# Optimization experiments

Hardware: AMD Instinct MI355X
Metric: run time of the kernel (lower is better)

## Reference

```python
import jax, jax.numpy as jnp
import numpy as np

B, L, D = 256, 256, 128          # batch, max_len, embedding_dim
H = W = 16                       # H=int(sqrt(L)), W=L//H
N, CBD = 128, 1024               # embedding_num, code_book_dim = N*8 = D*8
BETA = 0.25
BN_EPS = 1e-3                    # tf.layers.batch_normalization default


def _conv(x, w, b):
    return jax.lax.conv_general_dilated(x, w, (1, 1), 'VALID',
        dimension_numbers=('NHWC', 'HWIO', 'NHWC')) + b


def _convT(x, w, b):
    return jax.lax.conv_transpose(x, w, (1, 1), 'VALID',
        dimension_numbers=('NHWC', 'HWIO', 'NHWC')) + b


def _bn(x, g, b):
    # inference-mode BN with moving_mean=0, moving_var=1 (tf.layers default training=False)
    return g * (x * (1.0 / np.sqrt(1.0 + BN_EPS))) + b


def setup_inputs() -> dict:
    key = jax.random.key(0)
    ks = jax.random.split(key, 24)
    rn = lambda k, s, sc=0.05: (jax.random.normal(k, s, dtype=jnp.float32) * sc)
    inp = {
        'x': jax.random.normal(ks[0], (B, L, D), dtype=jnp.float32),
        'mask': jnp.ones((B, L), dtype=jnp.float32),
        'code_book': jax.random.normal(ks[1], (N, CBD), dtype=jnp.float32),
        # encoder: conv2d k=2 valid, channels D -> 2D -> 4D -> 8D
        'ew1': rn(ks[2], (2, 2, D, 2 * D)), 'eb1': jnp.zeros((2 * D,), jnp.float32),
        'eg1': jnp.ones((2 * D,), jnp.float32), 'ebt1': jnp.zeros((2 * D,), jnp.float32),
        'ew2': rn(ks[3], (2, 2, 2 * D, 4 * D)), 'eb2': jnp.zeros((4 * D,), jnp.float32),
        'eg2': jnp.ones((4 * D,), jnp.float32), 'ebt2': jnp.zeros((4 * D,), jnp.float32),
        'ew3': rn(ks[4], (2, 2, 4 * D, 8 * D)), 'eb3': jnp.zeros((8 * D,), jnp.float32),
        # decoder: conv2d_transpose k=2 valid, channels 8D -> 4D -> 2D -> D
        'dw1': rn(ks[5], (2, 2, 8 * D, 4 * D)), 'db1': jnp.zeros((4 * D,), jnp.float32),
        'dg1': jnp.ones((4 * D,), jnp.float32), 'dbt1': jnp.zeros((4 * D,), jnp.float32),
        'dw2': rn(ks[6], (2, 2, 4 * D, 2 * D)), 'db2': jnp.zeros((2 * D,), jnp.float32),
        'dg2': jnp.ones((2 * D,), jnp.float32), 'dbt2': jnp.zeros((2 * D,), jnp.float32),
        'dw3': rn(ks[7], (2, 2, 2 * D, D)), 'db3': jnp.zeros((D,), jnp.float32),
    }
    return inp


def reference(x, mask, code_book,
              ew1, eb1, eg1, ebt1, ew2, eb2, eg2, ebt2, ew3, eb3,
              dw1, db1, dg1, dbt1, dw2, db2, dg2, dbt2, dw3, db3):
    # ---- encoder (conv branch) ----
    xi = x.reshape(-1, H, W, D)                                   # [B,16,16,D]
    h = jax.nn.relu(_bn(_conv(xi, ew1, eb1), eg1, ebt1))          # [B,15,15,2D]
    h = jax.nn.relu(_bn(_conv(h, ew2, eb2), eg2, ebt2))           # [B,14,14,4D]
    x_encode = _conv(h, ew3, eb3)                                 # [B,13,13,8D]

    # ---- VQ codebook lookup (get_quantized) ----
    flat = x_encode.reshape(-1, CBD)                              # [B*169, CBD]
    dist = (jnp.sum(flat ** 2, axis=1, keepdims=True)
            + jnp.sum(code_book ** 2, axis=1)
            - 2.0 * flat @ code_book.T)                           # [B*169, N]
    idx = jnp.argmin(dist, axis=1)
    quantized = code_book[idx].reshape(x_encode.shape)            # gather == one_hot @ code_book

    # ---- straight-through + decoder ----
    ste = x_encode + jax.lax.stop_gradient(quantized - x_encode)
    h = jax.nn.relu(_bn(_convT(ste, dw1, db1), dg1, dbt1))        # [B,14,14,4D]
    h = jax.nn.relu(_bn(_convT(h, dw2, db2), dg2, dbt2))          # [B,15,15,2D]
    vq = _convT(h, dw3, db3)                                      # [B,16,16,D]
    vq_x = vq.reshape(-1, L, D)

    vq_mean = jnp.sum(vq_x, axis=1) / jnp.sum(mask, axis=-1, keepdims=True)

    recon = jnp.mean((x - vq_x) ** 2)
    vq_l = jnp.mean((quantized - jax.lax.stop_gradient(x_encode)) ** 2)
    commit = jnp.mean((x_encode - jax.lax.stop_gradient(quantized)) ** 2)
    vqvae_loss = recon + vq_l + BETA * commit
    return (vq_mean, vq_x, x_encode, quantized, vqvae_loss)
```

## Files before the change

### kernel.cpp

```cpp
#include <hip/hip_runtime.h>
#include <math.h>

typedef float f4 __attribute__((ext_vector_type(4)));
typedef short s8 __attribute__((ext_vector_type(8)));

#define WS_FLOATS 66000000L
__device__ float g_fallback[WS_FLOATS];

__device__ __forceinline__ f4 ldg4(const float* p) { return *(const f4*)p; }

__device__ __forceinline__ unsigned short bfr(float x) {
    unsigned int u = __float_as_uint(x);
    u += 0x7fffu + ((u >> 16) & 1u);
    return (unsigned short)(u >> 16);
}
__device__ __forceinline__ float bff(unsigned short h) {
    return __uint_as_float(((unsigned int)h) << 16);
}
__device__ __forceinline__ s8 z8() { s8 z = {0,0,0,0,0,0,0,0}; return z; }

__device__ __forceinline__ void split8(const f4& x0, const f4& x1, s8& hi, s8& lo) {
#pragma unroll
    for (int e = 0; e < 4; ++e) {
        unsigned short h0 = bfr(x0[e]);
        hi[e] = (short)h0; lo[e] = (short)bfr(x0[e] - bff(h0));
        unsigned short h1 = bfr(x1[e]);
        hi[e + 4] = (short)h1; lo[e + 4] = (short)bfr(x1[e] - bff(h1));
    }
}

template<int EPI>
__global__ __launch_bounds__(512, 2)
void gemm256(const short* __restrict__ aSrc, const short* __restrict__ wHi,
             const float* __restrict__ bias, const float* __restrict__ gamma,
             const float* __restrict__ beta, void* __restrict__ oHi,
             double* __restrict__ sacc, const short* __restrict__ zsrc,
             int IH, int IW, int OHOW, int OW, int N, int K, int off,
             int ntShift, float bns)
{
    extern __shared__ short smem[];

    const int tid = threadIdx.x;
    const int w = tid >> 6;
    const int l = tid & 63;
    const int lr = l >> 3;
    const int lc = l & 7;
    const int fr = l & 15, fq = l >> 4;
    const int wm = (w >> 2) * 128;
    const int wn = (w & 3) * 64;

    int m0, n0;
    {
        const int nwg = gridDim.x;
        const int bid = blockIdx.x;
        const int q = nwg >> 3, r = nwg & 7;
        const int xcd = bid & 7, c = bid >> 3;
        const int wg = (xcd < r ? xcd * (q + 1) : r * (q + 1) + (xcd - r) * q) + c;
        const int NTm1 = (1 << ntShift) - 1;
        m0 = (wg >> ntShift) * 256;
        n0 = (wg & NTm1) * 256;
    }

    int bOff[4], oiA[4], ojA[4], bRowB[4];
#pragma unroll
    for (int i = 0; i < 4; ++i) {
        int row = (w << 5) + (i << 3) + lr;
        int m = m0 + row;
        int b = m / OHOW; int rem = m - b * OHOW;
        oiA[i] = rem / OW; ojA[i] = rem - oiA[i] * OW;
        bOff[i] = b * IH * IW;
        bRowB[i] = (n0 + row) * K;
    }
    const int swz = (lc ^ lr) << 3;

    auto stage = [&](int sel, int kc) {
        short* Ab = smem + sel * 16384;
        short* Bb = smem + 32768 + sel * 16384;
        const int t = kc >> 9;
        const int ci = (kc & 511) + swz;
        const int di = (t >> 1) + off, dj = (t & 1) + off;
#pragma unroll
        for (int i = 0; i < 4; ++i) {
            int ii = oiA[i] + di, jj = ojA[i] + dj;
            bool v = (ii >= 0) && (ii < IH) && (jj >= 0) && (jj < IW);
            const short* sA = v ? aSrc + (long)(bOff[i] + ii * IW + jj) * 512 + ci
                                : zsrc + (l << 3);
            __builtin_amdgcn_global_load_lds(
                (const __attribute__((address_space(1))) void*)sA,
                (__attribute__((address_space(3))) void*)(Ab + (((w << 5) + (i << 3)) * 64)),
                16, 0, 0);
            const short* sB = wHi + bRowB[i] + kc + swz;
            __builtin_amdgcn_global_load_lds(
                (const __attribute__((address_space(1))) void*)sB,
                (__attribute__((address_space(3))) void*)(Bb + (((w << 5) + (i << 3)) * 64)),
                16, 0, 0);
        }
    };

    f4 acc[8][4];
#pragma unroll
    for (int a = 0; a < 8; ++a)
#pragma unroll
        for (int b = 0; b < 4; ++b) acc[a][b] = (f4){0.f, 0.f, 0.f, 0.f};

    const int NT = K >> 6;
    stage(0, 0);
    stage(1, 64);

    for (int t = 0; t < NT; ++t) {
        const int sel = t & 1;
        const short* Ab = smem + sel * 16384;
        const short* Bb = smem + 32768 + sel * 16384;

        if (t < NT - 1) asm volatile("s_waitcnt vmcnt(8)" ::: "memory");
        else            asm volatile("s_waitcnt vmcnt(0)" ::: "memory");
        __builtin_amdgcn_s_barrier();
        __builtin_amdgcn_sched_barrier(0);

        s8 af[8], bf[4];
#pragma unroll
        for (int mf = 0; mf < 8; ++mf) {
            int row = wm + mf * 16 + fr;
            int c = fq ^ (row & 7);
            af[mf] = *(const s8*)&Ab[row * 64 + (c << 3)];
        }
#pragma unroll
        for (int nf = 0; nf < 4; ++nf) {
            int row = wn + nf * 16 + fr;
            int c = fq ^ (row & 7);
            bf[nf] = *(const s8*)&Bb[row * 64 + (c << 3)];
        }
        asm volatile("s_waitcnt lgkmcnt(0)" ::: "memory");
        __builtin_amdgcn_sched_barrier(0);
        __builtin_amdgcn_s_setprio(1);
#pragma unroll
        for (int mf = 0; mf < 8; ++mf)
#pragma unroll
            for (int nf = 0; nf < 4; ++nf)
                acc[mf][nf] = __builtin_amdgcn_mfma_f32_16x16x32_bf16(
                    af[mf], bf[nf], acc[mf][nf], 0, 0, 0);
        __builtin_amdgcn_s_setprio(0);

#pragma unroll
        for (int mf = 0; mf < 8; ++mf) {
            int row = wm + mf * 16 + fr;
            int c = (4 + fq) ^ (row & 7);
            af[mf] = *(const s8*)&Ab[row * 64 + (c << 3)];
        }
#pragma unroll
        for (int nf = 0; nf < 4; ++nf) {
            int row = wn + nf * 16 + fr;
            int c = (4 + fq) ^ (row & 7);
            bf[nf] = *(const s8*)&Bb[row * 64 + (c << 3)];
        }
        asm volatile("s_waitcnt lgkmcnt(0)" ::: "memory");
        __builtin_amdgcn_sched_barrier(0);
        __builtin_amdgcn_s_barrier();
        __builtin_amdgcn_sched_barrier(0);
        if (t + 2 < NT) stage(sel, (t + 2) << 6);

        __builtin_amdgcn_s_setprio(1);
#pragma unroll
        for (int mf = 0; mf < 8; ++mf)
#pragma unroll
            for (int nf = 0; nf < 4; ++nf)
                acc[mf][nf] = __builtin_amdgcn_mfma_f32_16x16x32_bf16(
                    af[mf], bf[nf], acc[mf][nf], 0, 0, 0);
        __builtin_amdgcn_s_setprio(0);
    }

    if (EPI == 3) {
        float bi[4];
#pragma unroll
        for (int nf = 0; nf < 4; ++nf) bi[nf] = bias[n0 + wn + nf * 16 + fr];
        double tsum = 0.0;
#pragma unroll
        for (int mf = 0; mf < 8; ++mf)
#pragma unroll
            for (int j = 0; j < 4; ++j) {
                long gm = m0 + wm + mf * 16 + fq * 4 + j;
                float* orow = (float*)oHi + gm * (long)N + n0;
#pragma unroll
                for (int nf = 0; nf < 4; ++nf) {
                    float v = acc[mf][nf][j] + bi[nf];
                    orow[wn + nf * 16 + fr] = v;
                    tsum += (double)v * v;
                }
            }
        __syncthreads();
        double* rd = (double*)smem;
        rd[tid] = tsum; __syncthreads();
        for (int h = 256; h; h >>= 1) {
            if (tid < h) rd[tid] += rd[tid + h];
            __syncthreads();
        }
        if (tid == 0) atomicAdd(sacc, rd[0]);
    } else {
        float bi[4], ga[4], be[4];
#pragma unroll
        for (int nf = 0; nf < 4; ++nf) {
            int col = n0 + wn + nf * 16 + fr;
            bi[nf] = bias[col]; ga[nf] = gamma[col]; be[nf] = beta[col];
        }
#pragma unroll
        for (int mf = 0; mf < 8; ++mf)
#pragma unroll
            for (int j = 0; j < 4; ++j) {
                long gm = m0 + wm + mf * 16 + fq * 4 + j;
                short* orow = (short*)oHi + gm * (long)N + n0;
#pragma unroll
                for (int nf = 0; nf < 4; ++nf) {
                    float v = ga[nf] * ((acc[mf][nf][j] + bi[nf]) * bns) + be[nf];
                    orow[wn + nf * 16 + fr] = (short)bfr(fmaxf(v, 0.f));
                }
            }
    }
}

template<int SPLIT, int ASRC, int EPI, int OUTF>
__global__ __launch_bounds__(256, 2)
void mfma_conv(const void* __restrict__ aHi, const void* __restrict__ aLo,
               const short* __restrict__ wHi, const short* __restrict__ wLo,
               const float* __restrict__ bias, const float* __restrict__ gamma,
               const float* __restrict__ beta,
               void* __restrict__ oHi, void* __restrict__ oLo,
               int* __restrict__ idxo,
               const float* __restrict__ xref, float* __restrict__ colsum,
               double* __restrict__ sacc,
               int IH, int IW, int Cin, int cinShift, int OHOW, int OW,
               int N, int K, int off, int ntShift, float bns)
{
    constexpr int PL = 128 * 64;
    constexpr int NPL = (SPLIT == 1) ? 3 : 4;
    __shared__ short smem[NPL * PL];
    short* Ah = smem;
    short* Al  = smem + PL;
    short* BhS = smem + 2 * PL;
    short* BlS = smem + 3 * PL;

    const int tid = threadIdx.x;
    const int lane = tid & 63, wid = tid >> 6;
    const int fr = lane & 15, fq = lane >> 4;
    const int wm = (wid >> 1) * 64, wn = (wid & 1) * 64;

    int m0, n0;
    {
        const int nwg = gridDim.x;
        const int bid = blockIdx.x;
        const int q = nwg >> 3, r = nwg & 7;
        const int xcd = bid & 7, c = bid >> 3;
        const int wg = (xcd < r ? xcd * (q + 1) : r * (q + 1) + (xcd - r) * q) + c;
        const int NTm1 = (1 << ntShift) - 1;
        m0 = (wg >> ntShift) * 128;
        n0 = (wg & NTm1) * 128;
    }

    const int sr = tid >> 1;
    const int skh = (tid & 1) << 5;

    long tapOff[4]; bool tv[4];
    {
        int m = m0 + sr;
        int b = m / OHOW; int rem = m - b * OHOW;
        int oi = rem / OW; int oj = rem - oi * OW;
#pragma unroll
        for (int t = 0; t < 4; ++t) {
            int ii = oi + (t >> 1) + off, jj = oj + (t & 1) + off;
            bool v = (ii >= 0) && (ii < IH) && (jj >= 0) && (jj < IW);
            tv[t] = v;
            tapOff[t] = ((long)b * IH + (v ? ii : 0)) * IW + (v ? jj : 0);
        }
    }

    f4 acc[4][4];
#pragma unroll
    for (int a = 0; a < 4; ++a)
#pragma unroll
        for (int b = 0; b < 4; ++b) acc[a][b] = (f4){0.f, 0.f, 0.f, 0.f};

    const short* wHrow = wHi + (long)(n0 + sr) * K;
    const short* wLrow = (SPLIT == 2) ? (wLo + (long)(n0 + sr) * K) : nullptr;

    const int swzW = (sr & 7) << 3;
    const int sbase = sr * 64;

    s8 rah[4], ral[4], rbh[4], rbl[4];
    f4 rax0[4], rax1[4];

    auto LOADREGS = [&](int kc) {
        const int kk = kc + skh;
        const int t = kk >> cinShift;
        const int ci = kk & (Cin - 1);
        const bool v = tv[t];
        if (ASRC == 0) {
            const float* p = (const float*)aHi + tapOff[t] * Cin + ci;
#pragma unroll
            for (int q = 0; q < 4; ++q) {
                rax0[q] = v ? ldg4(p + 8 * q) : (f4){0.f,0.f,0.f,0.f};
                rax1[q] = v ? ldg4(p + 8 * q + 4) : (f4){0.f,0.f,0.f,0.f};
            }
        } else if (ASRC == 1) {
            const short* ph = (const short*)aHi + tapOff[t] * Cin + ci;
            const short* pl = (const short*)aLo + tapOff[t] * Cin + ci;
#pragma unroll
            for (int q = 0; q < 4; ++q) {
                rah[q] = v ? *(const s8*)(ph + 8 * q) : z8();
                ral[q] = v ? *(const s8*)(pl + 8 * q) : z8();
            }
        } else {
            const short* ph = (const short*)aHi + tapOff[t] * Cin + ci;
#pragma unroll
            for (int q = 0; q < 4; ++q) rah[q] = v ? *(const s8*)(ph + 8 * q) : z8();
        }
        if (SPLIT == 2) {
#pragma unroll
            for (int q = 0; q < 4; ++q) {
                rbh[q] = *(const s8*)(wHrow + kc + skh + 8 * q);
                rbl[q] = *(const s8*)(wLrow + kc + skh + 8 * q);
            }
        }
    };

    auto STORE = [&]() {
        if (ASRC == 0) {
#pragma unroll
            for (int q = 0; q < 4; ++q) split8(rax0[q], rax1[q], rah[q], ral[q]);
        }
#pragma unroll
        for (int q = 0; q < 4; ++q) {
            int kx = (skh + 8 * q) ^ swzW;
            *(s8*)&Ah[sbase + kx] = rah[q];
            if (SPLIT == 2) {
                *(s8*)&Al[sbase + kx]  = ral[q];
                *(s8*)&BhS[sbase + kx] = rbh[q];
                *(s8*)&BlS[sbase + kx] = rbl[q];
            }
        }
    };

    auto stageB = [&](int bsel, int kc2) {
        short* bb = smem + (1 + bsel) * PL;
        const int rr0 = wid << 5;
#pragma unroll
        for (int i = 0; i < 4; ++i) {
            const int r = rr0 + 8 * i + (lane >> 3);
            const int c = lane & 7;
            const short* src = wHi + (long)(n0 + r) * K + kc2 + 8 * (c ^ (r & 7));
            __builtin_amdgcn_global_load_lds(
                (const __attribute__((address_space(1))) void*)src,
                (__attribute__((address_space(3))) void*)(bb + (rr0 + 8 * i) * 64),
                16, 0, 0);
        }
    };

    int bcur = 0;
    LOADREGS(0);
    if (SPLIT == 1) stageB(0, 0);

    for (int kc = 0; kc < K; kc += 64) {
        if (SPLIT == 1) {
            asm volatile("s_waitcnt lgkmcnt(0)" ::: "memory");
            __builtin_amdgcn_s_barrier();
            STORE();
            if (kc + 64 < K) {
                stageB(bcur ^ 1, kc + 64);
                asm volatile("s_waitcnt vmcnt(4)" ::: "memory");
            } else {
                asm volatile("s_waitcnt vmcnt(0)" ::: "memory");
            }
            __builtin_amdgcn_sched_barrier(0);
            asm volatile("s_waitcnt lgkmcnt(0)" ::: "memory");
            __builtin_amdgcn_s_barrier();
        } else {
            __syncthreads();
            STORE();
            __syncthreads();
        }
        if (kc + 64 < K) LOADREGS(kc + 64);

        const short* Bc = (SPLIT == 1) ? (smem + (1 + bcur) * PL) : BhS;

        __builtin_amdgcn_s_setprio(1);
#pragma unroll
        for (int ks = 0; ks < 2; ++ks) {
            const int colk = ks * 32 + fq * 8;
            s8 afh[4], afl[4], bfh[4], bfl[4];
#pragma unroll
            for (int mf = 0; mf < 4; ++mf) {
                int ar = wm + mf * 16 + fr;
                int ai = ar * 64 + (colk ^ ((ar & 7) << 3));
                afh[mf] = *(const s8*)&Ah[ai];
                if (SPLIT == 2) afl[mf] = *(const s8*)&Al[ai];
            }
#pragma unroll
            for (int nf = 0; nf < 4; ++nf) {
                int br = wn + nf * 16 + fr;
                int bi2 = br * 64 + (colk ^ ((br & 7) << 3));
                bfh[nf] = *(const s8*)&Bc[bi2];
                if (SPLIT == 2) bfl[nf] = *(const s8*)&BlS[bi2];
            }
#pragma unroll
            for (int mf = 0; mf < 4; ++mf)
#pragma unroll
                for (int nf = 0; nf < 4; ++nf) {
                    acc[mf][nf] = __builtin_amdgcn_mfma_f32_16x16x32_bf16(
                        afh[mf], bfh[nf], acc[mf][nf], 0, 0, 0);
                    if (SPLIT == 2) {
                        acc[mf][nf] = __builtin_amdgcn_mfma_f32_16x16x32_bf16(
                            afh[mf], bfl[nf], acc[mf][nf], 0, 0, 0);
                        acc[mf][nf] = __builtin_amdgcn_mfma_f32_16x16x32_bf16(
                            afl[mf], bfh[nf], acc[mf][nf], 0, 0, 0);
                    }
                }
        }
        __builtin_amdgcn_s_setprio(0);
        bcur ^= 1;
    }

    if (EPI == 2) {
        __syncthreads();
        float* pbv = (float*)smem;
        int*   piv = (int*)((float*)smem + 256);
        float cnv[4];
#pragma unroll
        for (int nf = 0; nf < 4; ++nf) cnv[nf] = bias[n0 + wn + nf * 16 + fr];
#pragma unroll
        for (int mf = 0; mf < 4; ++mf)
#pragma unroll
            for (int j = 0; j < 4; ++j) {
                float best = 3.4e38f; int bi = 0;
#pragma unroll
                for (int nf = 0; nf < 4; ++nf) {
                    float d = cnv[nf] - 2.0f * acc[mf][nf][j];
                    int col = wn + nf * 16 + fr;
                    if (d < best) { best = d; bi = col; }
                }
#pragma unroll
                for (int sh = 1; sh <= 8; sh <<= 1) {
                    float ov = __shfl_xor(best, sh, 64);
                    int ob = __shfl_xor(bi, sh, 64);
                    if (ov < best || (ov == best && ob < bi)) { best = ov; bi = ob; }
                }
                if (fr == 0) {
                    int r = wm + mf * 16 + fq * 4 + j;
                    pbv[(wid & 1) * 128 + r] = best;
                    piv[(wid & 1) * 128 + r] = bi;
                }
            }
        __syncthreads();
        double win = 0.0;
        if (tid < 128) {
            float b0 = pbv[tid], b1 = pbv[128 + tid];
            int i0 = piv[tid], i1 = piv[128 + tid];
            idxo[m0 + tid] = (b1 < b0) ? i1 : i0;
            win = (double)((b1 < b0) ? b1 : b0);
        }
        __syncthreads();
        double* rd = (double*)smem;
        rd[tid] = win; __syncthreads();
        for (int h = 128; h; h >>= 1) {
            if (tid < h) rd[tid] += rd[tid + h];
            __syncthreads();
        }
        if (tid == 0) atomicAdd(sacc, rd[0]);
        return;
    }

    float bi[4], ga[4], be[4];
#pragma unroll
    for (int nf = 0; nf < 4; ++nf) {
        int col = n0 + wn + nf * 16 + fr;
        bi[nf] = bias[col];
        if (EPI == 1) { ga[nf] = gamma[col]; be[nf] = beta[col]; }
    }
    double tsum = 0.0;
    float csum[4] = {0.f, 0.f, 0.f, 0.f};
#pragma unroll
    for (int mf = 0; mf < 4; ++mf)
#pragma unroll
        for (int j = 0; j < 4; ++j) {
            long gm = m0 + wm + mf * 16 + fq * 4 + j;
#pragma unroll
            for (int nf = 0; nf < 4; ++nf) {
                int col = n0 + wn + nf * 16 + fr;
                float vv = acc[mf][nf][j] + bi[nf];
                if (EPI == 1) {
                    vv = ga[nf] * (vv * bns) + be[nf];
                    vv = fmaxf(vv, 0.f);
                }
                long o = gm * (long)N + col;
                if (OUTF == 0) {
                    ((float*)oHi)[o] = vv;
                } else if (OUTF == 2) {
                    ((short*)oHi)[o] = (short)bfr(vv);
                } else {
                    unsigned short h = bfr(vv);
                    ((short*)oHi)[o] = (short)h;
                    ((short*)oLo)[o] = (short)bfr(vv - bff(h));
                }
                if (EPI == 3) tsum += (double)vv * vv;
                if (EPI == 4) {
                    float d = vv - xref[o];
                    tsum += (double)d * d;
                    csum[nf] += vv;
                }
            }
        }
    if (EPI == 4) {
        int bb128 = (m0 >> 8) * 128;
#pragma unroll
        for (int nf = 0; nf < 4; ++nf)
            atomicAdd(&colsum[bb128 + n0 + wn + nf * 16 + fr], csum[nf]);
    }
    if (EPI == 3 || EPI == 4) {
        __syncthreads();
        double* rd = (double*)smem;
        rd[tid] = tsum; __syncthreads();
        for (int h = 128; h; h >>= 1) {
            if (tid < h) rd[tid] += rd[tid + h];
            __syncthreads();
        }
        if (tid == 0) atomicAdd(sacc, rd[0]);
    }
}

__global__ void prep_all(const float* __restrict__ ew1, const float* __restrict__ ew2,
                         const float* __restrict__ ew3, const float* __restrict__ dw1,
                         const float* __restrict__ dw2, const float* __restrict__ dw3,
                         const float* __restrict__ cb,
                         short* __restrict__ ewt1h, short* __restrict__ ewt1l,
                         short* __restrict__ ewt2h, short* __restrict__ ewt2l,
                         short* __restrict__ ewt3h,
                         short* __restrict__ dwt1Th, short* __restrict__ dwt1Tl,
                         short* __restrict__ dwt2h, short* __restrict__ dwt3h,
                         short* __restrict__ cbh, short* __restrict__ cbl,
                         float* __restrict__ zbuf)
{
    int b = blockIdx.x;
    int t = threadIdx.x;
    if (b < 512) {
        int i = b * 256 + t; int n = i >> 9, k = i & 511;
        float x = ew1[(long)k * 256 + n]; unsigned short h = bfr(x);
        ewt1h[i] = (short)h; ewt1l[i] = (short)bfr(x - bff(h));
    } else if (b < 2560) {
        int i = (b - 512) * 256 + t; int n = i >> 10, k = i & 1023;
        float x = ew2[(long)k * 512 + n]; unsigned short h = bfr(x);
        ewt2h[i] = (short)h; ewt2l[i] = (short)bfr(x - bff(h));
    } else if (b < 10752) {
        int i = (b - 2560) * 256 + t; int n = i >> 11, k = i & 2047;
        ewt3h[i] = (short)bfr(ew3[(long)k * 1024 + n]);
    } else if (b < 18944) {
        int i = (b - 10752) * 256 + t; int Np = i >> 10, co = i & 1023;
        int tt = Np >> 9, nn = Np & 511;
        float x = dw1[((long)(tt * 1024 + co)) * 512 + nn]; unsigned short h = bfr(x);
        dwt1Th[i] = (short)h; dwt1Tl[i] = (short)bfr(x - bff(h));
    } else if (b < 20992) {
        int i = (b - 18944) * 256 + t; int n = i >> 11, k = i & 2047;
        dwt2h[i] = (short)bfr(dw2[(long)k * 256 + n]);
    } else if (b < 21504) {
        int i = (b - 20992) * 256 + t; int n = i >> 10, k = i & 1023;
        dwt3h[i] = (short)bfr(dw3[(long)k * 128 + n]);
    } else if (b < 22016) {
        int i = (b - 21504) * 256 + t;
        float x = cb[i]; unsigned short h = bfr(x);
        cbh[i] = (short)h; cbl[i] = (short)bfr(x - bff(h));
    } else {
        int i = (b - 22016) * 256 + t; if (i < 2048) zbuf[i] = 0.f;
    }
}

__global__ void wsplitT(const float* __restrict__ p1, short* __restrict__ hi,
                        short* __restrict__ lo)
{
    int i = blockIdx.x * 256 + threadIdx.x;
    if (i >= 262144) return;
    int n = i >> 11, k = i & 2047;
    float x = p1[(long)k * 128 + n];
    unsigned short h = bfr(x);
    hi[i] = (short)h;
    lo[i] = (short)bfr(x - bff(h));
}

__global__ void code_bias(const float* __restrict__ cb, const float* __restrict__ eb3,
                          float* __restrict__ bias2)
{
    int c = blockIdx.x * 4 + (threadIdx.x >> 6);
    int lane = threadIdx.x & 63;
    if (c >= 128) return;
    const f4* p = (const f4*)(cb + (long)c * 1024);
    const f4* e = (const f4*)eb3;
    float s2 = 0.f, su = 0.f;
#pragma unroll
    for (int q = 0; q < 4; ++q) {
        f4 v = p[q * 64 + lane];
        f4 w = e[q * 64 + lane];
        s2 += (v[0]*v[0] + v[1]*v[1]) + (v[2]*v[2] + v[3]*v[3]);
        su += (v[0]*w[0] + v[1]*w[1]) + (v[2]*w[2] + v[3]*w[3]);
    }
#pragma unroll
    for (int sh = 32; sh; sh >>= 1) {
        s2 += __shfl_xor(s2, sh, 64);
        su += __shfl_xor(su, sh, 64);
    }
    if (lane == 0) bias2[c] = s2 - 2.f * su;
}

__global__ __launch_bounds__(256)
void d1_gather(const float* __restrict__ CD, const int* __restrict__ idx,
               const float* __restrict__ db1, const float* __restrict__ dg1,
               const float* __restrict__ dbt1, short* __restrict__ out, float bns)
{
    int m = blockIdx.x * 4 + (threadIdx.x >> 6);
    int lane = threadIdx.x & 63;
    if (m >= 50176) return;
    int b = m / 196, rem = m - b * 196;
    int oi = rem / 14, oj = rem - oi * 14;
    float2 acc[4];
#pragma unroll
    for (int q = 0; q < 4; ++q) acc[q] = make_float2(0.f, 0.f);
#pragma unroll
    for (int t = 0; t < 4; ++t) {
        int ii = oi - 1 + (t >> 1), jj = oj - 1 + (t & 1);
        if (ii >= 0 && ii < 13 && jj >= 0 && jj < 13) {
            int c = idx[(b * 13 + ii) * 13 + jj];
            const float2* p = (const float2*)(CD + ((long)c * 2048 + t * 512));
#pragma unroll
            for (int q = 0; q < 4; ++q) {
                float2 v = p[lane + 64 * q];
                acc[q].x += v.x; acc[q].y += v.y;
            }
        }
    }
#pragma unroll
    for (int q = 0; q < 4; ++q) {
        int n = 2 * (lane + 64 * q);
        float v0 = fmaxf(dg1[n]     * ((acc[q].x + db1[n])     * bns) + dbt1[n],     0.f);
        float v1 = fmaxf(dg1[n + 1] * ((acc[q].y + db1[n + 1]) * bns) + dbt1[n + 1], 0.f);
        short2 s2v;
        s2v.x = (short)bfr(v0); s2v.y = (short)bfr(v1);
        ((short2*)out)[(long)m * 256 + lane + 64 * q] = s2v;
    }
}

__global__ void gather_rows(const float* __restrict__ cb, const int* __restrict__ idx,
                            float* __restrict__ q)
{
    int m = blockIdx.x;
    int c = idx[m];
    const f4* src = (const f4*)(cb + (long)c * 1024);
    f4* dst = (f4*)(q + (long)m * 1024);
    dst[threadIdx.x] = src[threadIdx.x];
}

__global__ void finalize2(const double* __restrict__ s, float* __restrict__ loss)
{
    if (threadIdx.x == 0)
        loss[0] = (float)(s[0] / 8388608.0 + 1.25 * ((s[1] + s[2]) / 44302336.0));
}

__global__ void vq_mean_fin(const float* __restrict__ colsum,
                            const float* __restrict__ mask, float* __restrict__ o)
{
    __shared__ float red[128];
    int b = blockIdx.x;
    int d = threadIdx.x;
    red[d] = mask[b * 256 + d] + mask[b * 256 + 128 + d];
    __syncthreads();
    for (int h = 64; h; h >>= 1) { if (d < h) red[d] += red[d + h]; __syncthreads(); }
    o[b * 128 + d] = colsum[b * 128 + d] / red[0];
}

extern "C" void kernel_launch(void* const* d_in, const int* in_sizes, int n_in,
                              void* d_out, int out_size, void* d_ws, size_t ws_size,
                              hipStream_t stream)
{
    const float* x    = (const float*)d_in[0];
    const float* mask = (const float*)d_in[1];
    const float* cb   = (const float*)d_in[2];
    const float* ew1 = (const float*)d_in[3];
    const float* eb1 = (const float*)d_in[4];
    const float* eg1 = (const float*)d_in[5];
    const float* ebt1= (const float*)d_in[6];
    const float* ew2 = (const float*)d_in[7];
    const float* eb2 = (const float*)d_in[8];
    const float* eg2 = (const float*)d_in[9];
    const float* ebt2= (const float*)d_in[10];
    const float* ew3 = (const float*)d_in[11];
    const float* eb3 = (const float*)d_in[12];
    const float* dw1 = (const float*)d_in[13];
    const float* db1 = (const float*)d_in[14];
    const float* dg1 = (const float*)d_in[15];
    const float* dbt1= (const float*)d_in[16];
    const float* dw2 = (const float*)d_in[17];
    const float* db2 = (const float*)d_in[18];
    const float* dg2 = (const float*)d_in[19];
    const float* dbt2= (const float*)d_in[20];
    const float* dw3 = (const float*)d_in[21];
    const float* db3 = (const float*)d_in[22];

    float* out = (float*)d_out;
    float* o_vqmean = out;
    float* o_vqx    = out + 32768;
    float* o_xe     = out + 8421376;
    float* o_q      = out + 52723712;
    float* o_loss   = out + 97026048;

    float* base;
    if (ws_size >= (size_t)WS_FLOATS * 4) {
        base = (float*)d_ws;
    } else {
        void* p = nullptr;
        hipGetSymbolAddress(&p, HIP_SYMBOL(g_fallback));
        base = (float*)p;
    }

    float* cur = base;
    short* h1h = (short*)cur; cur += 7372800;
    short* h1l = (short*)cur; cur += 7372800;
    short* h2h = (short*)cur; cur += 12845056;
    short* h2l = (short*)cur; cur += 12845056;
    short* d1o = (short*)cur; cur += 12845056;
    short* d2o = (short*)cur; cur += 7372800;
    short* ewt1h = (short*)cur; cur += 65536;
    short* ewt1l = (short*)cur; cur += 65536;
    short* ewt2h = (short*)cur; cur += 262144;
    short* ewt2l = (short*)cur; cur += 262144;
    short* ewt3h = (short*)cur; cur += 1048576;
    short* dwt1Th = (short*)cur; cur += 1048576;
    short* dwt1Tl = (short*)cur; cur += 1048576;
    short* dwt2h = (short*)cur; cur += 262144;
    short* dwt3h = (short*)cur; cur += 65536;
    short* cbh   = (short*)cur; cur += 65536;
    short* cbl   = (short*)cur; cur += 65536;
    float* P1raw = cur; cur += 262144;
    short* wvh   = (short*)cur; cur += 131072;
    short* wvl   = (short*)cur; cur += 131072;
    float* CDt   = cur; cur += 262144;
    float* bias2 = cur; cur += 128;
    float* zbuf  = cur; cur += 2048;
    int* idxb = (int*)cur; cur += 43264;
    float* colsum = cur; cur += 32768;
    double* sdbl = (double*)cur; cur += 16;

    const float bns = (float)(1.0 / sqrt(1.0 + 1e-3));

    hipFuncSetAttribute(reinterpret_cast<const void*>(&gemm256<3>),
                        hipFuncAttributeMaxDynamicSharedMemorySize, 131072);
    hipFuncSetAttribute(reinterpret_cast<const void*>(&gemm256<1>),
                        hipFuncAttributeMaxDynamicSharedMemorySize, 131072);

    hipMemsetAsync(colsum, 0, 32768 * sizeof(float), stream);
    hipMemsetAsync(sdbl, 0, 3 * sizeof(double), stream);
    prep_all<<<22024, 256, 0, stream>>>(ew1, ew2, ew3, dw1, dw2, dw3, cb,
        ewt1h, ewt1l, ewt2h, ewt2l, ewt3h, dwt1Th, dwt1Tl, dwt2h, dwt3h,
        cbh, cbl, zbuf);
    code_bias<<<32, 256, 0, stream>>>(cb, eb3, bias2);

    mfma_conv<2, 0, 0, 0><<<16, 256, 0, stream>>>(
        ew3, nullptr, cbh, cbl, zbuf, nullptr, nullptr, P1raw, nullptr, nullptr,
        nullptr, nullptr, nullptr,
        2, 2050, 1024, 10, 2048, 2048, 128, 1024, 0, 0, bns);
    wsplitT<<<1024, 256, 0, stream>>>(P1raw, wvh, wvl);
    mfma_conv<2, 0, 0, 0><<<16, 256, 0, stream>>>(
        cb, nullptr, dwt1Th, dwt1Tl, zbuf, nullptr, nullptr, CDt, nullptr, nullptr,
        nullptr, nullptr, nullptr,
        2, 130, 1024, 10, 128, 128, 2048, 1024, 0, 4, bns);

    mfma_conv<2, 0, 1, 1><<<900, 256, 0, stream>>>(
        x, nullptr, ewt1h, ewt1l, eb1, eg1, ebt1, h1h, h1l, nullptr,
        nullptr, nullptr, nullptr,
        16, 16, 128, 7, 225, 15, 256, 512, 0, 1, bns);
    mfma_conv<2, 1, 1, 1><<<1568, 256, 0, stream>>>(
        h1h, h1l, ewt2h, ewt2l, eb2, eg2, ebt2, h2h, h2l, nullptr,
        nullptr, nullptr, nullptr,
        15, 15, 256, 8, 196, 14, 512, 1024, 0, 2, bns);
    gemm256<3><<<676, 512, 131072, stream>>>(
        h2h, ewt3h, eb3, nullptr, nullptr, o_xe, sdbl + 1, (const short*)zbuf,
        14, 14, 169, 13, 1024, 2048, 0, 2, bns);

    mfma_conv<2, 1, 2, 0><<<338, 256, 0, stream>>>(
        h2h, h2l, wvh, wvl, bias2, nullptr, nullptr, nullptr, nullptr, idxb,
        nullptr, nullptr, sdbl + 2,
        14, 14, 512, 9, 169, 13, 128, 2048, 0, 0, bns);
    gather_rows<<<43264, 256, 0, stream>>>(cb, idxb, o_q);

    d1_gather<<<12544, 256, 0, stream>>>(CDt, idxb, db1, dg1, dbt1, d1o, bns);
    gemm256<1><<<225, 512, 131072, stream>>>(
        d1o, dwt2h, db2, dg2, dbt2, d2o, nullptr, (const short*)zbuf,
        14, 14, 225, 15, 256, 2048, -1, 0, bns);
    mfma_conv<1, 2, 4, 0><<<512, 256, 0, stream>>>(
        d2o, nullptr, dwt3h, nullptr, db3, nullptr, nullptr, o_vqx, nullptr, nullptr,
        x, colsum, sdbl + 0,
        15, 15, 256, 8, 256, 16, 128, 1024, -1, 0, bns);

    vq_mean_fin<<<256, 128, 0, stream>>>(colsum, mask, o_vqmean);
    finalize2<<<1, 64, 0, stream>>>(sdbl, o_loss);
}
```

Measured before the change: 901.4 us.

## Replace encoder conv2 with dedicated 256x128-tile split-bf16 GEMM kernel

Encoder layer-2 conv (256->512 channels, 2x2) moves from the generic mfma_conv path to a specialized e2_gemm kernel. It uses 512-thread blocks with 256x128 output tiles, double-buffered global_load_lds staging with XOR swizzle, XCD-aware block remapping, and three-term hi/lo bf16 MFMA for near-fp32 accuracy. The aim is more data reuse per tile and better overlap of loads with MFMA. In exchange it uses a large shared-memory footprint and hardcodes the layer shapes.

```diff
diff --git a/kernel.cpp b/kernel.cpp
--- a/kernel.cpp
+++ b/kernel.cpp
@@ -27,6 +27,147 @@
         unsigned short h1 = bfr(x1[e]);
         hi[e + 4] = (short)h1; lo[e + 4] = (short)bfr(x1[e] - bff(h1));
     }
+}
+
+__global__ __launch_bounds__(512, 2)
+void e2_gemm(const short* __restrict__ aHi, const short* __restrict__ aLo,
+             const short* __restrict__ wHi, const short* __restrict__ wLo,
+             const float* __restrict__ bias, const float* __restrict__ gamma,
+             const float* __restrict__ beta,
+             short* __restrict__ oHi, short* __restrict__ oLo, float bns)
+{
+    extern __shared__ short smem[];
+    const int tid = threadIdx.x;
+    const int w = tid >> 6, l = tid & 63;
+    const int fr = l & 15, fq = l >> 4;
+    const int wm = (w >> 2) * 128;
+    const int wn = (w & 3) * 32;
+
+    int m0, n0;
+    {
+        const int nwg = gridDim.x;
+        const int bid = blockIdx.x;
+        const int q = nwg >> 3, r = nwg & 7;
+        const int xcd = bid & 7, c = bid >> 3;
+        const int wg = (xcd < r ? xcd * (q + 1) : r * (q + 1) + (xcd - r) * q) + c;
+        m0 = (wg >> 2) * 256;
+        n0 = (wg & 3) * 128;
+    }
+
+    int aBase[2], aSwz[2], aDst[2];
+#pragma unroll
+    for (int i = 0; i < 2; ++i) {
+        int p = tid + 512 * i;
+        int row = p >> 2, ch = p & 3;
+        int m = m0 + row;
+        int b = m / 196; int rem = m - b * 196;
+        int oi = rem / 14, oj = rem - oi * 14;
+        aBase[i] = ((b * 15 + oi) * 15 + oj) * 256;
+        aSwz[i] = (ch ^ (row & 3)) << 3;
+        aDst[i] = row * 32 + ch * 8;
+    }
+    const int bRow = tid >> 2, bch = tid & 3;
+    const int bSrcO = (n0 + bRow) * 1024 + ((bch ^ (bRow & 3)) << 3);
+    const int bDst = bRow * 32 + bch * 8;
+
+    auto stage = [&](int sel, int kc) {
+        const int t = kc >> 8;
+        const int toff = ((t >> 1) * 15 + (t & 1)) * 256 + (kc & 255);
+#pragma unroll
+        for (int i = 0; i < 2; ++i) {
+            __builtin_amdgcn_global_load_lds(
+                (const __attribute__((address_space(1))) void*)(aHi + aBase[i] + toff + aSwz[i]),
+                (__attribute__((address_space(3))) void*)(smem + sel * 8192 + aDst[i]), 16, 0, 0);
+            __builtin_amdgcn_global_load_lds(
+                (const __attribute__((address_space(1))) void*)(aLo + aBase[i] + toff + aSwz[i]),
+                (__attribute__((address_space(3))) void*)(smem + 16384 + sel * 8192 + aDst[i]), 16, 0, 0);
+        }
+        __builtin_amdgcn_global_load_lds(
+            (const __attribute__((address_space(1))) void*)(wHi + bSrcO + kc),
+            (__attribute__((address_space(3))) void*)(smem + 32768 + sel * 4096 + bDst), 16, 0, 0);
+        __builtin_amdgcn_global_load_lds(
+            (const __attribute__((address_space(1))) void*)(wLo + bSrcO + kc),
+            (__attribute__((address_space(3))) void*)(smem + 40960 + sel * 4096 + bDst), 16, 0, 0);
+    };
+
+    f4 acc[8][2];
+#pragma unroll
+    for (int a = 0; a < 8; ++a)
+#pragma unroll
+        for (int b = 0; b < 2; ++b) acc[a][b] = (f4){0.f, 0.f, 0.f, 0.f};
+
+    stage(0, 0);
+    stage(1, 32);
+
+    for (int t = 0; t < 32; ++t) {
+        const int sel = t & 1;
+        if (t < 31) asm volatile("s_waitcnt vmcnt(6)" ::: "memory");
+        else        asm volatile("s_waitcnt vmcnt(0)" ::: "memory");
+        __builtin_amdgcn_s_barrier();
+        __builtin_amdgcn_sched_barrier(0);
+
+        const short* Ah = smem + sel * 8192;
+        const short* Al = smem + 16384 + sel * 8192;
+        const short* Bh = smem + 32768 + sel * 4096;
+        const short* Bl = smem + 40960 + sel * 4096;
+
+        s8 afh[8], afl[8], bfh[2], bfl[2];
+#pragma unroll
+        for (int mf = 0; mf < 8; ++mf) {
+            int ar = wm + mf * 16 + fr;
+            int ao = ar * 32 + ((fq ^ (ar & 3)) << 3);
+            afh[mf] = *(const s8*)&Ah[ao];
+            afl[mf] = *(const s8*)&Al[ao];
+        }
+#pragma unroll
+        for (int nf = 0; nf < 2; ++nf) {
+            int br = wn + nf * 16 + fr;
+            int bo = br * 32 + ((fq ^ (br & 3)) << 3);
+            bfh[nf] = *(const s8*)&Bh[bo];
+            bfl[nf] = *(const s8*)&Bl[bo];
+        }
+        asm volatile("s_waitcnt lgkmcnt(0)" ::: "memory");
+        __builtin_amdgcn_sched_barrier(0);
+        __builtin_amdgcn_s_barrier();
+        __builtin_amdgcn_sched_barrier(0);
+        if (t + 2 < 32) stage(sel, (t + 2) * 32);
+
+        __builtin_amdgcn_s_setprio(1);
+#pragma unroll
+        for (int mf = 0; mf < 8; ++mf)
+#pragma unroll
+            for (int nf = 0; nf < 2; ++nf) {
+                acc[mf][nf] = __builtin_amdgcn_mfma_f32_16x16x32_bf16(
+                    afh[mf], bfh[nf], acc[mf][nf], 0, 0, 0);
+                acc[mf][nf] = __builtin_amdgcn_mfma_f32_16x16x32_bf16(
+                    afh[mf], bfl[nf], acc[mf][nf], 0, 0, 0);
+                acc[mf][nf] = __builtin_amdgcn_mfma_f32_16x16x32_bf16(
+                    afl[mf], bfh[nf], acc[mf][nf], 0, 0, 0);
+            }
+        __builtin_amdgcn_s_setprio(0);
+    }
+
+    float bi2[2], ga[2], be[2];
+#pragma unroll
+    for (int nf = 0; nf < 2; ++nf) {
+        int col = n0 + wn + nf * 16 + fr;
+        bi2[nf] = bias[col]; ga[nf] = gamma[col]; be[nf] = beta[col];
+    }
+#pragma unroll
+    for (int mf = 0; mf < 8; ++mf)
+#pragma unroll
+        for (int j = 0; j < 4; ++j) {
+            long gm = m0 + wm + mf * 16 + fq * 4 + j;
+#pragma unroll
+            for (int nf = 0; nf < 2; ++nf) {
+                float v = ga[nf] * ((acc[mf][nf][j] + bi2[nf]) * bns) + be[nf];
+                v = fmaxf(v, 0.f);
+                long o = gm * 512 + n0 + wn + nf * 16 + fr;
+                unsigned short h = bfr(v);
+                oHi[o] = (short)h;
+                oLo[o] = (short)bfr(v - bff(h));
+            }
+        }
 }
 
 template<int EPI>
@@ -748,6 +889,8 @@
                         hipFuncAttributeMaxDynamicSharedMemorySize, 131072);
     hipFuncSetAttribute(reinterpret_cast<const void*>(&gemm256<1>),
                         hipFuncAttributeMaxDynamicSharedMemorySize, 131072);
+    hipFuncSetAttribute(reinterpret_cast<const void*>(&e2_gemm),
+                        hipFuncAttributeMaxDynamicSharedMemorySize, 98304);
 
     hipMemsetAsync(colsum, 0, 32768 * sizeof(float), stream);
     hipMemsetAsync(sdbl, 0, 3 * sizeof(double), stream);
@@ -770,10 +913,8 @@
         x, nullptr, ewt1h, ewt1l, eb1, eg1, ebt1, h1h, h1l, nullptr,
         nullptr, nullptr, nullptr,
         16, 16, 128, 7, 225, 15, 256, 512, 0, 1, bns);
-    mfma_conv<2, 1, 1, 1><<<1568, 256, 0, stream>>>(
-        h1h, h1l, ewt2h, ewt2l, eb2, eg2, ebt2, h2h, h2l, nullptr,
-        nullptr, nullptr, nullptr,
-        15, 15, 256, 8, 196, 14, 512, 1024, 0, 2, bns);
+    e2_gemm<<<784, 512, 98304, stream>>>(
+        h1h, h1l, ewt2h, ewt2l, eb2, eg2, ebt2, h2h, h2l, bns);
     gemm256<3><<<676, 512, 131072, stream>>>(
         h2h, ewt3h, eb3, nullptr, nullptr, o_xe, sdbl + 1, (const short*)zbuf,
         14, 14, 169, 13, 1024, 2048, 0, 2, bns);
```

Result: slower. 939.4 us (+4.2%).
